# Kernel tuning notes

Hardware: AMD Instinct MI355X
Metric: run time of the kernel (lower is better)

Reference implementation:

```python
import jax, jax.numpy as jnp
import numpy as np

B, S, DIM = 8, 4096, 1024
DIM_LATENT = 1024
DEPTH = 2
NUM_LATENTS = 64
MAX_SEQ = 4096
DIM_HEAD = 64
HEADS = max(max(DIM, DIM_LATENT) // DIM_HEAD, 1)  # 16
INNER = HEADS * DIM_HEAD                           # 1024
HIDDEN = 4 * DIM_LATENT
LN_EPS = 1e-5
RMS_EPS = 1e-8


def setup_inputs() -> dict:
    key = jax.random.key(0)
    ks = jax.random.split(key, 10)
    return {
        "x": jax.random.normal(ks[0], (B, S, DIM), jnp.float32),
        "mask": jnp.ones((B, S), dtype=bool),
        "pos_table": jax.random.normal(ks[1], (MAX_SEQ, DIM), jnp.float32) * 0.02,
        "latents0": jax.random.normal(ks[2], (NUM_LATENTS, DIM_LATENT), jnp.float32) * 0.02,
        "ln_x_g": jnp.ones((DEPTH, DIM), jnp.float32),
        "ln_x_b": jnp.zeros((DEPTH, DIM), jnp.float32),
        "ln_l_g": jnp.ones((DEPTH, DIM_LATENT), jnp.float32),
        "ln_l_b": jnp.zeros((DEPTH, DIM_LATENT), jnp.float32),
        "qn_g": jnp.ones((DEPTH, DIM_HEAD), jnp.float32),
        "kn_g": jnp.ones((DEPTH, DIM_HEAD), jnp.float32),
        "Wq": jax.random.normal(ks[3], (DEPTH, DIM_LATENT, INNER), jnp.float32) * 0.02,
        "Wkv": jax.random.normal(ks[4], (DEPTH, DIM, 2 * INNER), jnp.float32) * 0.02,
        "Wo": jax.random.normal(ks[5], (DEPTH, INNER, DIM_LATENT), jnp.float32) * 0.02,
        "bo": jnp.zeros((DEPTH, DIM_LATENT), jnp.float32),
        "ff_ln_g": jnp.ones((DEPTH, DIM_LATENT), jnp.float32),
        "ff_ln_b": jnp.zeros((DEPTH, DIM_LATENT), jnp.float32),
        "W1": jax.random.normal(ks[6], (DEPTH, DIM_LATENT, HIDDEN), jnp.float32) * 0.02,
        "b1": jnp.zeros((DEPTH, HIDDEN), jnp.float32),
        "W2": jax.random.normal(ks[7], (DEPTH, HIDDEN, DIM_LATENT), jnp.float32) * 0.02,
        "b2": jnp.zeros((DEPTH, DIM_LATENT), jnp.float32),
        "fn_g": jnp.ones((DIM_LATENT,), jnp.float32),
        "fn_b": jnp.zeros((DIM_LATENT,), jnp.float32),
    }


def _ln(x, g, b):
    m = jnp.mean(x, axis=-1, keepdims=True)
    v = jnp.mean(jnp.square(x - m), axis=-1, keepdims=True)
    return (x - m) * jax.lax.rsqrt(v + LN_EPS) * g + b


def _rms(x, g):
    # torch RMSNorm: x / clamp(||x|| * d^-0.5, eps) * gamma
    n = jnp.sqrt(jnp.sum(jnp.square(x), axis=-1, keepdims=True)) * (DIM_HEAD ** -0.5)
    return x / jnp.maximum(n, RMS_EPS) * g


def reference(x, mask, pos_table, latents0, ln_x_g, ln_x_b, ln_l_g, ln_l_b,
              qn_g, kn_g, Wq, Wkv, Wo, bo, ff_ln_g, ff_ln_b, W1, b1, W2, b2,
              fn_g, fn_b):
    b, s, _ = x.shape
    x = x + pos_table[:s][None]                       # abs pos emb
    lat = jnp.broadcast_to(latents0, (b, NUM_LATENTS, DIM_LATENT))
    scale = DIM_HEAD ** -0.5
    pad_mask = jnp.concatenate(
        [mask, jnp.ones((b, NUM_LATENTS), dtype=bool)], axis=1)  # [b, s+nl]
    for i in range(DEPTH):
        xn = _ln(x, ln_x_g[i], ln_x_b[i])
        ln_lat = _ln(lat, ln_l_g[i], ln_l_b[i])
        # queries from latents
        q = (ln_lat @ Wq[i]).reshape(b, NUM_LATENTS, HEADS, DIM_HEAD)
        q = q.transpose(0, 2, 1, 3)                   # b h i d
        # kv from context + latents (dim == dim_latent -> shared to_kv)
        kv = jnp.concatenate([xn @ Wkv[i], ln_lat @ Wkv[i]], axis=1)
        n_kv = s + NUM_LATENTS
        kv = kv.reshape(b, n_kv, 2, HEADS, DIM_HEAD)
        k = kv[:, :, 0].transpose(0, 2, 1, 3)         # b h j d
        v = kv[:, :, 1].transpose(0, 2, 1, 3)
        sim = jnp.einsum('bhid,bhjd->bhij', _rms(q, qn_g[i]) * scale,
                         _rms(k, kn_g[i]))
        neg = -jnp.finfo(sim.dtype).max
        sim = jnp.where(pad_mask[:, None, None, :], sim, neg)
        attn = jax.nn.softmax(sim.astype(jnp.float32), axis=-1).astype(sim.dtype)
        out = jnp.einsum('bhij,bhjd->bhid', attn, v)
        out = out.transpose(0, 2, 1, 3).reshape(b, NUM_LATENTS, INNER)
        lat = out @ Wo[i] + bo[i] + lat               # attn residual
        h = _ln(lat, ff_ln_g[i], ff_ln_b[i]) @ W1[i] + b1[i]
        lat = jax.nn.gelu(h, approximate=False) @ W2[i] + b2[i] + lat  # ff residual
    return _ln(lat, fn_g, fn_b)
```

## Files before the change

### kernel.cpp

```cpp
#include <hip/hip_runtime.h>
#include <cstdint>
#include <cstddef>

typedef __bf16 bf16_t;
typedef __bf16 bf16x8 __attribute__((ext_vector_type(8)));
typedef float  f32x4  __attribute__((ext_vector_type(4)));

#define LN_EPS_F 1e-5f
#define RMS_EPS_F 1e-8f

static __device__ __forceinline__ void async_load16(const void* src, void* dst_lds) {
  __builtin_amdgcn_global_load_lds(
      (__attribute__((address_space(1))) void*)src,
      (__attribute__((address_space(3))) void*)dst_lds, 16, 0, 0);
}

static __device__ __forceinline__ unsigned short f2bfu(float f) {
  union { bf16_t h; unsigned short u; } cv;
  cv.h = (bf16_t)f;
  return cv.u;
}

__global__ __launch_bounds__(256)
void wconv_kernel(const float* __restrict__ src, bf16_t* __restrict__ dst, int K, int N) {
  __shared__ float t[32][33];
  int k0 = blockIdx.x * 32, n0 = blockIdx.y * 32;
  int tx = threadIdx.x & 31, ty = threadIdx.x >> 5;
  for (int r = ty; r < 32; r += 8)
    t[r][tx] = src[(size_t)(k0 + r) * N + n0 + tx];
  __syncthreads();
  for (int r = ty; r < 32; r += 8)
    dst[(size_t)(n0 + r) * K + k0 + tx] = (bf16_t)t[tx][r];
}

__global__ __launch_bounds__(256)
void ln_kernel(const float* __restrict__ X, const float* __restrict__ pos,
               const float* __restrict__ g, const float* __restrict__ bb,
               void* __restrict__ outp, int out_bf16) {
  int row = blockIdx.x, tid = threadIdx.x;
  int lane = tid & 63, wave = tid >> 6;
  float4 v = *(const float4*)(X + (size_t)row * 1024 + tid * 4);
  if (pos) {
    float4 p = *(const float4*)(pos + (size_t)(row & 4095) * 1024 + tid * 4);
    v.x += p.x; v.y += p.y; v.z += p.z; v.w += p.w;
  }
  float s1 = v.x + v.y + v.z + v.w;
  float s2 = v.x * v.x + v.y * v.y + v.z * v.z + v.w * v.w;
  for (int off = 32; off > 0; off >>= 1) {
    s1 += __shfl_xor(s1, off);
    s2 += __shfl_xor(s2, off);
  }
  __shared__ float red1[4], red2[4];
  if (lane == 0) { red1[wave] = s1; red2[wave] = s2; }
  __syncthreads();
  float S1 = red1[0] + red1[1] + red1[2] + red1[3];
  float S2 = red2[0] + red2[1] + red2[2] + red2[3];
  float mean = S1 * (1.0f / 1024.0f);
  float var  = S2 * (1.0f / 1024.0f) - mean * mean;
  float inv  = rsqrtf(var + LN_EPS_F);
  float4 gg  = *(const float4*)(g + tid * 4);
  float4 bb4 = *(const float4*)(bb + tid * 4);
  float y0 = (v.x - mean) * inv * gg.x + bb4.x;
  float y1 = (v.y - mean) * inv * gg.y + bb4.y;
  float y2 = (v.z - mean) * inv * gg.z + bb4.z;
  float y3 = (v.w - mean) * inv * gg.w + bb4.w;
  if (out_bf16) {
    ushort4 u; u.x = f2bfu(y0); u.y = f2bfu(y1); u.z = f2bfu(y2); u.w = f2bfu(y3);
    *(ushort4*)((bf16_t*)outp + (size_t)row * 1024 + tid * 4) = u;
  } else {
    float4 o; o.x = y0; o.y = y1; o.z = y2; o.w = y3;
    *(float4*)((float*)outp + (size_t)row * 1024 + tid * 4) = o;
  }
}

#define BAR() do { asm volatile("" ::: "memory"); __builtin_amdgcn_s_barrier(); asm volatile("" ::: "memory"); } while (0)
#define VMW(n_) asm volatile("s_waitcnt vmcnt(" #n_ ")" ::: "memory")

__global__ __launch_bounds__(512, 2)
void gemm256_kv(const bf16_t* __restrict__ A, const bf16_t* __restrict__ Bt,
                bf16_t* __restrict__ kbuf, bf16_t* __restrict__ vt,
                float* __restrict__ knsc, int K) {
  __shared__ __align__(16) bf16_t smem[65536];
  const int tid = threadIdx.x;
  const int lane = tid & 63, wave = tid >> 6;
  const int l15 = lane & 15, quad = lane >> 4;
  const int orig = blockIdx.x;
  const int xcd = orig & 7, pp_ = orig >> 3;
  const int m0 = (xcd * 16 + (pp_ >> 3)) * 256;
  const int n0 = (pp_ & 7) * 256;
  const int wm = (wave >> 2) * 128, wn = (wave & 3) * 64;

  const int r0 = wave * 16 + (lane >> 2);
  const int c0 = ((lane & 3) - (r0 >> 1)) & 3;
  const bf16_t* gA = A + (size_t)(m0 + r0) * K + c0 * 8;
  const bf16_t* gB = Bt + (size_t)(n0 + r0) * K + c0 * 8;

#define STG(t_, slot_) do {                                                    \
    const bf16_t* a_ = gA + (size_t)(t_) * 32;                                 \
    const bf16_t* b_ = gB + (size_t)(t_) * 32;                                 \
    bf16_t* d_ = smem + (slot_) * 16384 + wave * 512;                          \
    async_load16(a_, d_);                                                      \
    async_load16(a_ + (size_t)128 * K, d_ + 4096);                             \
    async_load16(b_, d_ + 8192);                                               \
    async_load16(b_ + (size_t)128 * K, d_ + 12288);                            \
  } while (0)

  const int rot = ((quad + (l15 >> 1)) & 3) << 3;
  const int offA0 = (wm + l15) * 32 + rot;
  const int offB0 = 8192 + (wn + l15) * 32 + rot;

  f32x4 acc[8][4];
  const f32x4 zero = {0.f, 0.f, 0.f, 0.f};
#pragma unroll
  for (int i = 0; i < 8; ++i)
#pragma unroll
    for (int j = 0; j < 4; ++j) acc[i][j] = zero;

  bf16x8 a[8], b[4], c[4];

#define ITER(t_, CUR, NXT) do {                                                \
    { int ts_ = (t_) + 3; if (ts_ > KT - 1) ts_ = KT - 1;                      \
      STG(ts_, ts_ & 3); }                                                     \
    const bf16_t* ns_ = smem + (((t_) + 1) & 3) * 16384;                       \
    _Pragma("unroll")                                                          \
    for (int mi = 0; mi < 8; ++mi) {                                           \
      _Pragma("unroll")                                                        \
      for (int ni = 0; ni < 4; ++ni)                                           \
        acc[mi][ni] = __builtin_amdgcn_mfma_f32_16x16x32_bf16(a[mi], CUR[ni], acc[mi][ni], 0, 0, 0); \
      a[mi] = *(const bf16x8*)(ns_ + offA0 + mi * 512);                        \
      if (mi < 4) NXT[mi] = *(const bf16x8*)(ns_ + offB0 + mi * 512);          \
    }                                                                          \
    VMW(4); BAR();                                                             \
  } while (0)

#define FCOMP(CUR) do {                                                        \
    _Pragma("unroll")                                                          \
    for (int mi = 0; mi < 8; ++mi)                                             \
      _Pragma("unroll")                                                        \
      for (int ni = 0; ni < 4; ++ni)                                           \
        acc[mi][ni] = __builtin_amdgcn_mfma_f32_16x16x32_bf16(a[mi], CUR[ni], acc[mi][ni], 0, 0, 0); \
  } while (0)

  const int KT = K >> 5;
  STG(0, 0); STG(1, 1); STG(2, 2);
  VMW(4); BAR();
#pragma unroll
  for (int mi = 0; mi < 8; ++mi) a[mi] = *(const bf16x8*)(smem + offA0 + mi * 512);
#pragma unroll
  for (int ni = 0; ni < 4; ++ni) b[ni] = *(const bf16x8*)(smem + offB0 + ni * 512);

  int t = 0;
  for (; t + 1 < KT - 1; t += 2) {
    ITER(t, b, c);
    ITER(t + 1, c, b);
  }
  ITER(t, b, c);
  FCOMP(c);
  __syncthreads();

  const int bq = m0 >> 12;
  const bool is_v = (n0 >= 1024);
  const int colbase = is_v ? (n0 - 1024) : n0;
  const int h = (colbase + wn) >> 6;
  const int bh = bq * 16 + h;
  const int j0w = (m0 & 4095) + wm;
  bf16_t* bnc = smem + wave * 8192;

  if (!is_v) {
#pragma unroll
    for (int mi = 0; mi < 8; ++mi) {
#pragma unroll
      for (int rg = 0; rg < 4; ++rg) {
        float tt = acc[mi][0][rg] * acc[mi][0][rg] + acc[mi][1][rg] * acc[mi][1][rg]
                 + acc[mi][2][rg] * acc[mi][2][rg] + acc[mi][3][rg] * acc[mi][3][rg];
        tt += __shfl_xor(tt, 1); tt += __shfl_xor(tt, 2);
        tt += __shfl_xor(tt, 4); tt += __shfl_xor(tt, 8);
        if (l15 == 0) {
          int jj = j0w + mi * 16 + quad * 4 + rg;
          knsc[(size_t)bh * 4160 + jj] = 1.0f / fmaxf(sqrtf(tt) * 0.125f, RMS_EPS_F);
        }
      }
    }
#pragma unroll
    for (int mi = 0; mi < 8; ++mi)
#pragma unroll
      for (int ni = 0; ni < 4; ++ni)
#pragma unroll
        for (int rg = 0; rg < 4; ++rg)
          bnc[(mi * 16 + quad * 4 + rg) * 64 + ni * 16 + l15] = (bf16_t)acc[mi][ni][rg];
#pragma unroll
    for (int p = 0; p < 16; ++p) {
      int e = p * 64 + lane;
      int jr = e >> 3, cq = e & 7;
      bf16x8 vl = *(const bf16x8*)&bnc[jr * 64 + cq * 8];
      *(bf16x8*)(kbuf + ((size_t)bh * 4160 + j0w + jr) * 64 + cq * 8) = vl;
    }
  } else {
#pragma unroll
    for (int mi = 0; mi < 8; ++mi)
#pragma unroll
      for (int ni = 0; ni < 4; ++ni) {
        ushort4 u;
        u.x = f2bfu(acc[mi][ni].x); u.y = f2bfu(acc[mi][ni].y);
        u.z = f2bfu(acc[mi][ni].z); u.w = f2bfu(acc[mi][ni].w);
        *(ushort4*)&bnc[(ni * 16 + l15) * 128 + mi * 16 + quad * 4] = u;
      }
#pragma unroll
    for (int p = 0; p < 16; ++p) {
      int e = p * 64 + lane;
      int dr = e >> 4, cq = e & 15;
      bf16x8 vl = *(const bf16x8*)&bnc[dr * 128 + cq * 8];
      *(bf16x8*)(vt + ((size_t)bh * 64 + dr) * 4160 + j0w + cq * 8) = vl;
    }
  }
#undef STG
#undef ITER
#undef FCOMP
}

__global__ __launch_bounds__(256)
void gemm64_bt(const bf16_t* __restrict__ A, const bf16_t* __restrict__ Bt,
               float* __restrict__ C, int K, int lda, int ldb, int ldc,
               int zdiv, long long aO, long long aI, long long bO, long long bI,
               long long cO, long long cI) {
  __shared__ __align__(16) bf16_t As[64 * 32];
  __shared__ __align__(16) bf16_t Bs[64 * 32];
  const int tid = threadIdx.x;
  const int lane = tid & 63, wave = tid >> 6;
  const int z = blockIdx.z;
  const int zh = z / zdiv, zl = z - zh * zdiv;
  const bf16_t* Ab = A + zh * aO + zl * aI;
  const bf16_t* Bb = Bt + zh * bO + zl * bI;
  float* Cb = C + zh * cO + zl * cI;
  const int m0 = blockIdx.x * 64, n0 = blockIdx.y * 64;
  const int wm = (wave >> 1) * 32, wn = (wave & 1) * 32;
  const int l15 = lane & 15, quad = lane >> 4;

  f32x4 acc[2][2];
  const f32x4 zero = {0.f, 0.f, 0.f, 0.f};
  acc[0][0] = zero; acc[0][1] = zero; acc[1][0] = zero; acc[1][1] = zero;

  const int ebase = wave * 64;
  const int e = ebase + lane;
  const int row = e >> 2, c = e & 3;
  for (int kb = 0; kb < K; kb += 32) {
    async_load16(Ab + (size_t)(m0 + row) * lda + kb + c * 8, &As[ebase * 8]);
    async_load16(Bb + (size_t)(n0 + row) * ldb + kb + c * 8, &Bs[ebase * 8]);
    __syncthreads();
    bf16x8 a0 = *(const bf16x8*)&As[(wm + l15) * 32 + quad * 8];
    bf16x8 a1 = *(const bf16x8*)&As[(wm + 16 + l15) * 32 + quad * 8];
    bf16x8 b0 = *(const bf16x8*)&Bs[(wn + l15) * 32 + quad * 8];
    bf16x8 b1 = *(const bf16x8*)&Bs[(wn + 16 + l15) * 32 + quad * 8];
    acc[0][0] = __builtin_amdgcn_mfma_f32_16x16x32_bf16(a0, b0, acc[0][0], 0, 0, 0);
    acc[0][1] = __builtin_amdgcn_mfma_f32_16x16x32_bf16(a0, b1, acc[0][1], 0, 0, 0);
    acc[1][0] = __builtin_amdgcn_mfma_f32_16x16x32_bf16(a1, b0, acc[1][0], 0, 0, 0);
    acc[1][1] = __builtin_amdgcn_mfma_f32_16x16x32_bf16(a1, b1, acc[1][1], 0, 0, 0);
    __syncthreads();
  }
#pragma unroll
  for (int mi = 0; mi < 2; ++mi) {
    int r0 = m0 + wm + mi * 16 + quad * 4;
#pragma unroll
    for (int ni = 0; ni < 2; ++ni) {
      int col = n0 + wn + ni * 16 + l15;
      float* p = Cb + (size_t)r0 * ldc + col;
      p[0] = acc[mi][ni].x;
      p[(size_t)ldc] = acc[mi][ni].y;
      p[(size_t)ldc * 2] = acc[mi][ni].z;
      p[(size_t)ldc * 3] = acc[mi][ni].w;
    }
  }
}

__global__ __launch_bounds__(256)
void rms_q_kernel(const float* __restrict__ q, const float* __restrict__ gq,
                  const float* __restrict__ gk, bf16_t* __restrict__ outp) {
  int gw = blockIdx.x * 4 + (threadIdx.x >> 6);
  int lane = threadIdx.x & 63;
  float x = q[(size_t)gw * 64 + lane];
  float ss = x * x;
  for (int off = 32; off > 0; off >>= 1) ss += __shfl_xor(ss, off);
  float n = sqrtf(ss) * 0.125f;
  outp[(size_t)gw * 64 + lane] =
      (bf16_t)(x / fmaxf(n, RMS_EPS_F) * gq[lane] * gk[lane] * 0.125f);
}

__global__ __launch_bounds__(256)
void prep_lat_kernel(const float* __restrict__ kvlat, float* __restrict__ knsc,
                     bf16_t* __restrict__ kbuf, bf16_t* __restrict__ vt) {
  int gw = blockIdx.x * 4 + (threadIdx.x >> 6);
  int lane = threadIdx.x & 63;
  int rowi = gw >> 4, h = gw & 15;
  int b = rowi >> 6, il = rowi & 63;
  float kx = kvlat[(size_t)rowi * 2048 + h * 64 + lane];
  float vx = kvlat[(size_t)rowi * 2048 + 1024 + h * 64 + lane];
  float ss = kx * kx;
  for (int off = 32; off > 0; off >>= 1) ss += __shfl_xor(ss, off);
  int bh = b * 16 + h, j = 4096 + il;
  kbuf[((size_t)bh * 4160 + j) * 64 + lane] = (bf16_t)kx;
  if (lane == 0)
    knsc[(size_t)bh * 4160 + j] = 1.0f / fmaxf(sqrtf(ss) * 0.125f, RMS_EPS_F);
  vt[((size_t)bh * 64 + lane) * 4160 + j] = (bf16_t)vx;
}

__global__ __launch_bounds__(256)
void flash_kernel(const bf16_t* __restrict__ qrms, const bf16_t* __restrict__ kbuf,
                  const bf16_t* __restrict__ vt, const float* __restrict__ knsc,
                  float* __restrict__ Opart, float* __restrict__ mpart,
                  float* __restrict__ lpart) {
  __shared__ __align__(16) bf16_t Qs[4096];
  __shared__ __align__(16) bf16_t Ks[4096];
  __shared__ __align__(16) bf16_t Vs[4096];
  __shared__ __align__(16) bf16_t Ps[4 * 16 * 72];
  __shared__ float kss[64];
  const int tid = threadIdx.x, lane = tid & 63, wave = tid >> 6;
  const int l15 = lane & 15, quad = lane >> 4;
  const int bh = blockIdx.z, ch = blockIdx.x;
  const int b = bh >> 4, h = bh & 15;

#pragma unroll
  for (int p = 0; p < 2; ++p) {
    int eb = p * 256 + wave * 64;
    int e = eb + lane;
    int i = e >> 3, q = e & 7;
    async_load16(qrms + (size_t)b * 65536 + (size_t)i * 1024 + h * 64 + ((q ^ (i & 7)) * 8),
                 &Qs[eb * 8]);
  }
  __syncthreads();
  bf16x8 qf[2];
#pragma unroll
  for (int kk = 0; kk < 2; ++kk)
    qf[kk] = *(const bf16x8*)&Qs[(wave * 16 + l15) * 64 + (((kk * 4 + quad) ^ (l15 & 7)) * 8)];

  float m_i[4], l_i[4];
  f32x4 O[4];
  const f32x4 zero = {0.f, 0.f, 0.f, 0.f};
#pragma unroll
  for (int rg = 0; rg < 4; ++rg) { m_i[rg] = -3.0e38f; l_i[rg] = 0.f; }
#pragma unroll
  for (int nd = 0; nd < 4; ++nd) O[nd] = zero;

  for (int t = 0; t < 5; ++t) {
    const int j0 = ch * 320 + t * 64;
    __syncthreads();
#pragma unroll
    for (int p = 0; p < 2; ++p) {
      int eb = p * 256 + wave * 64;
      int e = eb + lane;
      int rj = e >> 3, q = e & 7;
      async_load16(kbuf + ((size_t)bh * 4160 + j0 + rj) * 64 + ((q ^ (rj & 7)) * 8),
                   &Ks[eb * 8]);
      async_load16(vt + ((size_t)bh * 64 + rj) * 4160 + j0 + ((q ^ (rj & 7)) * 8),
                   &Vs[eb * 8]);
    }
    if (tid < 64) kss[tid] = knsc[(size_t)bh * 4160 + j0 + tid];
    __syncthreads();

    f32x4 s[4];
#pragma unroll
    for (int ni = 0; ni < 4; ++ni) s[ni] = zero;
#pragma unroll
    for (int kk = 0; kk < 2; ++kk) {
#pragma unroll
      for (int ni = 0; ni < 4; ++ni) {
        bf16x8 bv = *(const bf16x8*)&Ks[(ni * 16 + l15) * 64 + (((kk * 4 + quad) ^ (l15 & 7)) * 8)];
        s[ni] = __builtin_amdgcn_mfma_f32_16x16x32_bf16(qf[kk], bv, s[ni], 0, 0, 0);
      }
    }
#pragma unroll
    for (int ni = 0; ni < 4; ++ni) {
      float cs = kss[ni * 16 + l15];
      s[ni].x *= cs; s[ni].y *= cs; s[ni].z *= cs; s[ni].w *= cs;
    }
    float al[4];
#pragma unroll
    for (int rg = 0; rg < 4; ++rg) {
      float tm = fmaxf(fmaxf(s[0][rg], s[1][rg]), fmaxf(s[2][rg], s[3][rg]));
      tm = fmaxf(tm, __shfl_xor(tm, 1)); tm = fmaxf(tm, __shfl_xor(tm, 2));
      tm = fmaxf(tm, __shfl_xor(tm, 4)); tm = fmaxf(tm, __shfl_xor(tm, 8));
      float mn = fmaxf(m_i[rg], tm);
      al[rg] = __expf(m_i[rg] - mn);
      m_i[rg] = mn;
    }
    float rs[4] = {0.f, 0.f, 0.f, 0.f};
#pragma unroll
    for (int ni = 0; ni < 4; ++ni) {
#pragma unroll
      for (int rg = 0; rg < 4; ++rg) {
        float pv = __expf(s[ni][rg] - m_i[rg]);
        s[ni][rg] = pv;
        rs[rg] += pv;
        Ps[wave * 1152 + (quad * 4 + rg) * 72 + ni * 16 + l15] = (bf16_t)pv;
      }
    }
#pragma unroll
    for (int rg = 0; rg < 4; ++rg) {
      float t2 = rs[rg];
      t2 += __shfl_xor(t2, 1); t2 += __shfl_xor(t2, 2);
      t2 += __shfl_xor(t2, 4); t2 += __shfl_xor(t2, 8);
      l_i[rg] = l_i[rg] * al[rg] + t2;
    }
#pragma unroll
    for (int nd = 0; nd < 4; ++nd) {
      O[nd].x *= al[0]; O[nd].y *= al[1]; O[nd].z *= al[2]; O[nd].w *= al[3];
    }
#pragma unroll
    for (int kk2 = 0; kk2 < 2; ++kk2) {
      bf16x8 af = *(const bf16x8*)&Ps[wave * 1152 + l15 * 72 + kk2 * 32 + quad * 8];
#pragma unroll
      for (int nd = 0; nd < 4; ++nd) {
        bf16x8 bv = *(const bf16x8*)&Vs[(nd * 16 + l15) * 64 + (((kk2 * 4 + quad) ^ (l15 & 7)) * 8)];
        O[nd] = __builtin_amdgcn_mfma_f32_16x16x32_bf16(af, bv, O[nd], 0, 0, 0);
      }
    }
  }
  const size_t obase = (size_t)(ch * 128 + bh) * 64;
#pragma unroll
  for (int nd = 0; nd < 4; ++nd) {
    int colb = nd * 16 + l15;
#pragma unroll
    for (int rg = 0; rg < 4; ++rg) {
      int rowi = wave * 16 + quad * 4 + rg;
      Opart[(obase + rowi) * 64 + colb] = O[nd][rg];
    }
  }
  if (l15 == 0) {
#pragma unroll
    for (int rg = 0; rg < 4; ++rg) {
      int rowi = wave * 16 + quad * 4 + rg;
      mpart[obase + rowi] = m_i[rg];
      lpart[obase + rowi] = l_i[rg];
    }
  }
}

__global__ __launch_bounds__(256)
void combine_kernel(const float* __restrict__ Opart, const float* __restrict__ mpart,
                    const float* __restrict__ lpart, bf16_t* __restrict__ obf) {
  const int bh = blockIdx.z, xi = blockIdx.x;
  const int wave = threadIdx.x >> 6, lane = threadIdx.x & 63;
  const int b = bh >> 4, h = bh & 15;
  for (int ii = 0; ii < 4; ++ii) {
    int i = xi * 16 + ii * 4 + wave;
    float mv[13];
    float M = -3.0e38f;
#pragma unroll
    for (int c = 0; c < 13; ++c) {
      mv[c] = mpart[(size_t)(c * 128 + bh) * 64 + i];
      M = fmaxf(M, mv[c]);
    }
    float L = 0.f, acc = 0.f;
#pragma unroll
    for (int c = 0; c < 13; ++c) {
      float e = __expf(mv[c] - M);
      L += e * lpart[(size_t)(c * 128 + bh) * 64 + i];
      acc += e * Opart[((size_t)(c * 128 + bh) * 64 + i) * 64 + lane];
    }
    obf[(size_t)b * 65536 + (size_t)i * 1024 + h * 64 + lane] = (bf16_t)(acc / L);
  }
}

__global__ __launch_bounds__(256)
void lat_init_kernel(const float* __restrict__ l0, float* __restrict__ lat) {
  size_t i = (size_t)blockIdx.x * 256 + threadIdx.x;
  lat[i] = l0[i & 65535];
}
__global__ __launch_bounds__(256)
void resid_kernel(float* __restrict__ lat, const float* __restrict__ add,
                  const float* __restrict__ bias) {
  size_t i = (size_t)blockIdx.x * 256 + threadIdx.x;
  lat[i] += add[i] + bias[i & 1023];
}
__global__ __launch_bounds__(256)
void resid4_kernel(float* __restrict__ lat, const float* __restrict__ cs,
                   const float* __restrict__ bias) {
  size_t i = (size_t)blockIdx.x * 256 + threadIdx.x;
  lat[i] += bias[i & 1023] + cs[i] + cs[i + 524288] + cs[i + 1048576] + cs[i + 1572864];
}
__global__ __launch_bounds__(256)
void gelu_kernel(const float* __restrict__ h, const float* __restrict__ b1,
                 bf16_t* __restrict__ o) {
  size_t i = (size_t)blockIdx.x * 256 + threadIdx.x;
  float x = h[i] + b1[i & 4095];
  o[i] = (bf16_t)(0.5f * x * (1.0f + erff(x * 0.70710678118654752f)));
}

extern "C" void kernel_launch(void* const* d_in, const int* in_sizes, int n_in,
                              void* d_out, int out_size, void* d_ws, size_t ws_size,
                              hipStream_t stream) {
  const float* x      = (const float*)d_in[0];
  const float* pos    = (const float*)d_in[2];
  const float* lat0   = (const float*)d_in[3];
  const float* ln_x_g = (const float*)d_in[4];
  const float* ln_x_b = (const float*)d_in[5];
  const float* ln_l_g = (const float*)d_in[6];
  const float* ln_l_b = (const float*)d_in[7];
  const float* qn_g   = (const float*)d_in[8];
  const float* kn_g   = (const float*)d_in[9];
  const float* Wq     = (const float*)d_in[10];
  const float* Wkv    = (const float*)d_in[11];
  const float* Wo     = (const float*)d_in[12];
  const float* bo     = (const float*)d_in[13];
  const float* ffln_g = (const float*)d_in[14];
  const float* ffln_b = (const float*)d_in[15];
  const float* W1     = (const float*)d_in[16];
  const float* b1     = (const float*)d_in[17];
  const float* W2     = (const float*)d_in[18];
  const float* b2     = (const float*)d_in[19];
  const float* fn_g   = (const float*)d_in[20];
  const float* fn_b   = (const float*)d_in[21];
  (void)in_sizes; (void)n_in; (void)out_size; (void)ws_size;

  char* base = (char*)d_ws;
  size_t off = 0;
  auto alloc = [&](size_t bytes) -> void* {
    void* p = base + off;
    off += (bytes + 255) & ~(size_t)255;
    return p;
  };
  bf16_t* Wqt   = (bf16_t*)alloc(2ull * 1024 * 1024 * 2);
  bf16_t* Wkvt  = (bf16_t*)alloc(2ull * 2048 * 1024 * 2);
  bf16_t* Wot   = (bf16_t*)alloc(2ull * 1024 * 1024 * 2);
  bf16_t* W1t   = (bf16_t*)alloc(2ull * 4096 * 1024 * 2);
  bf16_t* W2t   = (bf16_t*)alloc(2ull * 1024 * 4096 * 2);
  bf16_t* xn    = (bf16_t*)alloc(32768ull * 1024 * 2);
  bf16_t* kbuf  = (bf16_t*)alloc(128ull * 4160 * 64 * 2);
  bf16_t* vt    = (bf16_t*)alloc(128ull * 64 * 4160 * 2);
  float*  knsc  = (float*)alloc(128ull * 4160 * 4);
  float*  Opart = (float*)alloc(13ull * 128 * 64 * 64 * 4);
  float*  mpart = (float*)alloc(13ull * 128 * 64 * 4);
  float*  lpart = (float*)alloc(13ull * 128 * 64 * 4);
  float*  lat   = (float*)alloc(512ull * 1024 * 4);
  bf16_t* lnl   = (bf16_t*)alloc(512ull * 1024 * 2);
  float*  qbuf  = (float*)alloc(512ull * 1024 * 4);
  bf16_t* qrms  = (bf16_t*)alloc(512ull * 1024 * 2);
  float*  kvlat = (float*)alloc(512ull * 2048 * 4);
  bf16_t* obf   = (bf16_t*)alloc(512ull * 1024 * 2);
  float*  oW    = (float*)alloc(512ull * 1024 * 4);
  float*  ffh   = (float*)alloc(512ull * 4096 * 4);
  bf16_t* ffgb  = (bf16_t*)alloc(512ull * 4096 * 2);
  float*  ffo   = (float*)alloc(512ull * 1024 * 4);
  (void)ffo;

  for (int i = 0; i < 2; ++i) {
    wconv_kernel<<<dim3(32, 32), 256, 0, stream>>>(Wq  + (size_t)i * 1024 * 1024, Wqt  + (size_t)i * 1024 * 1024, 1024, 1024);
    wconv_kernel<<<dim3(32, 64), 256, 0, stream>>>(Wkv + (size_t)i * 1024 * 2048, Wkvt + (size_t)i * 2048 * 1024, 1024, 2048);
    wconv_kernel<<<dim3(32, 32), 256, 0, stream>>>(Wo  + (size_t)i * 1024 * 1024, Wot  + (size_t)i * 1024 * 1024, 1024, 1024);
    wconv_kernel<<<dim3(32, 128), 256, 0, stream>>>(W1 + (size_t)i * 1024 * 4096, W1t + (size_t)i * 4096 * 1024, 1024, 4096);
    wconv_kernel<<<dim3(128, 32), 256, 0, stream>>>(W2 + (size_t)i * 4096 * 1024, W2t + (size_t)i * 1024 * 4096, 4096, 1024);
  }
  lat_init_kernel<<<2048, 256, 0, stream>>>(lat0, lat);

  for (int i = 0; i < 2; ++i) {
    ln_kernel<<<32768, 256, 0, stream>>>(x, pos, ln_x_g + i * 1024, ln_x_b + i * 1024, xn, 1);
    gemm256_kv<<<dim3(1024), dim3(512), 0, stream>>>(xn, Wkvt + (size_t)i * 2048 * 1024, kbuf, vt, knsc, 1024);
    ln_kernel<<<512, 256, 0, stream>>>(lat, nullptr, ln_l_g + i * 1024, ln_l_b + i * 1024, lnl, 1);
    gemm64_bt<<<dim3(8, 16, 1), 256, 0, stream>>>(lnl, Wqt + (size_t)i * 1024 * 1024, qbuf,
        1024, 1024, 1024, 1024, 1, 0, 0, 0, 0, 0, 0);
    gemm64_bt<<<dim3(8, 32, 1), 256, 0, stream>>>(lnl, Wkvt + (size_t)i * 2048 * 1024, kvlat,
        1024, 1024, 1024, 2048, 1, 0, 0, 0, 0, 0, 0);
    rms_q_kernel<<<2048, 256, 0, stream>>>(qbuf, qn_g + i * 64, kn_g + i * 64, qrms);
    prep_lat_kernel<<<2048, 256, 0, stream>>>(kvlat, knsc, kbuf, vt);
    flash_kernel<<<dim3(13, 1, 128), 256, 0, stream>>>(qrms, kbuf, vt, knsc, Opart, mpart, lpart);
    combine_kernel<<<dim3(4, 1, 128), 256, 0, stream>>>(Opart, mpart, lpart, obf);
    gemm64_bt<<<dim3(8, 16, 1), 256, 0, stream>>>(obf, Wot + (size_t)i * 1024 * 1024, oW,
        1024, 1024, 1024, 1024, 1, 0, 0, 0, 0, 0, 0);
    resid_kernel<<<2048, 256, 0, stream>>>(lat, oW, bo + i * 1024);
    ln_kernel<<<512, 256, 0, stream>>>(lat, nullptr, ffln_g + i * 1024, ffln_b + i * 1024, lnl, 1);
    gemm64_bt<<<dim3(8, 64, 1), 256, 0, stream>>>(lnl, W1t + (size_t)i * 4096 * 1024, ffh,
        1024, 1024, 1024, 4096, 1, 0, 0, 0, 0, 0, 0);
    gelu_kernel<<<8192, 256, 0, stream>>>(ffh, b1 + i * 4096, ffgb);
    gemm64_bt<<<dim3(8, 16, 4), 256, 0, stream>>>(ffgb, W2t + (size_t)i * 1024 * 4096, ffh,
        1024, 4096, 4096, 1024, 4, 0, 1024, 0, 1024, 0, 524288);
    resid4_kernel<<<2048, 256, 0, stream>>>(lat, ffh, b2 + i * 1024);
  }
  ln_kernel<<<512, 256, 0, stream>>>(lat, nullptr, fn_g, fn_b, d_out, 0);
}
```

Before: 1.035 ms.

## Load KV GEMM B operand straight from global into registers, halve LDS

The KV projection GEMM now stages only the A tile through LDS. Each wave loads its B fragments directly from global memory into registers one k-step ahead, and the pipeline is restructured around this. The change halves shared memory per block, and the epilogue is split into two halves with an XOR-swizzled LDS layout to fit the smaller buffer and avoid bank conflicts. In exchange, B is fetched redundantly from global by the waves that share it, and global-load latency for B is now exposed more directly.

```diff
diff --git a/kernel.cpp b/kernel.cpp
--- a/kernel.cpp
+++ b/kernel.cpp
@@ -80,7 +80,7 @@
 void gemm256_kv(const bf16_t* __restrict__ A, const bf16_t* __restrict__ Bt,
                 bf16_t* __restrict__ kbuf, bf16_t* __restrict__ vt,
                 float* __restrict__ knsc, int K) {
-  __shared__ __align__(16) bf16_t smem[65536];
+  __shared__ __align__(16) bf16_t smem[32768];
   const int tid = threadIdx.x;
   const int lane = tid & 63, wave = tid >> 6;
   const int l15 = lane & 15, quad = lane >> 4;
@@ -93,21 +93,24 @@
   const int r0 = wave * 16 + (lane >> 2);
   const int c0 = ((lane & 3) - (r0 >> 1)) & 3;
   const bf16_t* gA = A + (size_t)(m0 + r0) * K + c0 * 8;
-  const bf16_t* gB = Bt + (size_t)(n0 + r0) * K + c0 * 8;
 
 #define STG(t_, slot_) do {                                                    \
     const bf16_t* a_ = gA + (size_t)(t_) * 32;                                 \
-    const bf16_t* b_ = gB + (size_t)(t_) * 32;                                 \
-    bf16_t* d_ = smem + (slot_) * 16384 + wave * 512;                          \
+    bf16_t* d_ = smem + (slot_) * 8192 + wave * 512;                           \
     async_load16(a_, d_);                                                      \
     async_load16(a_ + (size_t)128 * K, d_ + 4096);                             \
-    async_load16(b_, d_ + 8192);                                               \
-    async_load16(b_ + (size_t)128 * K, d_ + 12288);                            \
   } while (0)
 
   const int rot = ((quad + (l15 >> 1)) & 3) << 3;
   const int offA0 = (wm + l15) * 32 + rot;
-  const int offB0 = 8192 + (wn + l15) * 32 + rot;
+
+  const bf16_t* gBf = Bt + (size_t)(n0 + wn + l15) * K + quad * 8;
+
+#define BLD(t_, R_) do {                                                       \
+    _Pragma("unroll")                                                          \
+    for (int ni = 0; ni < 4; ++ni)                                             \
+      R_[ni] = *(const bf16x8*)(gBf + (size_t)ni * 16 * K + (size_t)(t_) * 32);\
+  } while (0)
 
   f32x4 acc[8][4];
   const f32x4 zero = {0.f, 0.f, 0.f, 0.f};
@@ -118,22 +121,10 @@
 
   bf16x8 a[8], b[4], c[4];
 
-#define ITER(t_, CUR, NXT) do {                                                \
-    { int ts_ = (t_) + 3; if (ts_ > KT - 1) ts_ = KT - 1;                      \
-      STG(ts_, ts_ & 3); }                                                     \
-    const bf16_t* ns_ = smem + (((t_) + 1) & 3) * 16384;                       \
+#define COMP(slot_, CUR) do {                                                  \
+    const bf16_t* sb_ = smem + (slot_) * 8192;                                 \
     _Pragma("unroll")                                                          \
-    for (int mi = 0; mi < 8; ++mi) {                                           \
-      _Pragma("unroll")                                                        \
-      for (int ni = 0; ni < 4; ++ni)                                           \
-        acc[mi][ni] = __builtin_amdgcn_mfma_f32_16x16x32_bf16(a[mi], CUR[ni], acc[mi][ni], 0, 0, 0); \
-      a[mi] = *(const bf16x8*)(ns_ + offA0 + mi * 512);                        \
-      if (mi < 4) NXT[mi] = *(const bf16x8*)(ns_ + offB0 + mi * 512);          \
-    }                                                                          \
-    VMW(4); BAR();                                                             \
-  } while (0)
-
-#define FCOMP(CUR) do {                                                        \
+    for (int mi = 0; mi < 8; ++mi) a[mi] = *(const bf16x8*)(sb_ + offA0 + mi * 512); \
     _Pragma("unroll")                                                          \
     for (int mi = 0; mi < 8; ++mi)                                             \
       _Pragma("unroll")                                                        \
@@ -141,13 +132,19 @@
         acc[mi][ni] = __builtin_amdgcn_mfma_f32_16x16x32_bf16(a[mi], CUR[ni], acc[mi][ni], 0, 0, 0); \
   } while (0)
 
+#define ITER(t_, CUR, NXT) do {                                                \
+    BLD((t_) + 1, NXT);                                                        \
+    { int ts_ = (t_) + 3; if (ts_ > KT - 1) ts_ = KT - 1;                      \
+      STG(ts_, ((t_) + 3) & 3); }                                              \
+    COMP((t_) & 3, CUR);                                                       \
+    __builtin_amdgcn_sched_barrier(0);                                         \
+    VMW(8); BAR();                                                             \
+  } while (0)
+
   const int KT = K >> 5;
   STG(0, 0); STG(1, 1); STG(2, 2);
+  BLD(0, b);
   VMW(4); BAR();
-#pragma unroll
-  for (int mi = 0; mi < 8; ++mi) a[mi] = *(const bf16x8*)(smem + offA0 + mi * 512);
-#pragma unroll
-  for (int ni = 0; ni < 4; ++ni) b[ni] = *(const bf16x8*)(smem + offB0 + ni * 512);
 
   int t = 0;
   for (; t + 1 < KT - 1; t += 2) {
@@ -155,7 +152,7 @@
     ITER(t + 1, c, b);
   }
   ITER(t, b, c);
-  FCOMP(c);
+  COMP((KT - 1) & 3, c);
   __syncthreads();
 
   const int bq = m0 >> 12;
@@ -164,7 +161,7 @@
   const int h = (colbase + wn) >> 6;
   const int bh = bq * 16 + h;
   const int j0w = (m0 & 4095) + wm;
-  bf16_t* bnc = smem + wave * 8192;
+  bf16_t* bnc = smem + wave * 4096;
 
   if (!is_v) {
 #pragma unroll
@@ -182,40 +179,60 @@
       }
     }
 #pragma unroll
-    for (int mi = 0; mi < 8; ++mi)
-#pragma unroll
-      for (int ni = 0; ni < 4; ++ni)
-#pragma unroll
-        for (int rg = 0; rg < 4; ++rg)
-          bnc[(mi * 16 + quad * 4 + rg) * 64 + ni * 16 + l15] = (bf16_t)acc[mi][ni][rg];
-#pragma unroll
-    for (int p = 0; p < 16; ++p) {
-      int e = p * 64 + lane;
-      int jr = e >> 3, cq = e & 7;
-      bf16x8 vl = *(const bf16x8*)&bnc[jr * 64 + cq * 8];
-      *(bf16x8*)(kbuf + ((size_t)bh * 4160 + j0w + jr) * 64 + cq * 8) = vl;
+    for (int half = 0; half < 2; ++half) {
+      if (half) __syncthreads();
+#pragma unroll
+      for (int mi = 0; mi < 4; ++mi) {
+        int mg = half * 4 + mi;
+#pragma unroll
+        for (int ni = 0; ni < 4; ++ni) {
+          int g = ni * 2 + (l15 >> 3);
+#pragma unroll
+          for (int rg = 0; rg < 4; ++rg) {
+            int j = mi * 16 + quad * 4 + rg;
+            bnc[j * 64 + (((g ^ (j & 7)) << 3) | (l15 & 7))] = (bf16_t)acc[mg][ni][rg];
+          }
+        }
+      }
+#pragma unroll
+      for (int p = 0; p < 8; ++p) {
+        int e = p * 64 + lane;
+        int jr = e >> 3, cq = e & 7;
+        bf16x8 vl = *(const bf16x8*)&bnc[jr * 64 + ((cq ^ (jr & 7)) << 3)];
+        *(bf16x8*)(kbuf + ((size_t)bh * 4160 + j0w + half * 64 + jr) * 64 + cq * 8) = vl;
+      }
     }
   } else {
 #pragma unroll
-    for (int mi = 0; mi < 8; ++mi)
-#pragma unroll
-      for (int ni = 0; ni < 4; ++ni) {
-        ushort4 u;
-        u.x = f2bfu(acc[mi][ni].x); u.y = f2bfu(acc[mi][ni].y);
-        u.z = f2bfu(acc[mi][ni].z); u.w = f2bfu(acc[mi][ni].w);
-        *(ushort4*)&bnc[(ni * 16 + l15) * 128 + mi * 16 + quad * 4] = u;
-      }
-#pragma unroll
-    for (int p = 0; p < 16; ++p) {
-      int e = p * 64 + lane;
-      int dr = e >> 4, cq = e & 15;
-      bf16x8 vl = *(const bf16x8*)&bnc[dr * 128 + cq * 8];
-      *(bf16x8*)(vt + ((size_t)bh * 64 + dr) * 4160 + j0w + cq * 8) = vl;
+    for (int half = 0; half < 2; ++half) {
+      if (half) __syncthreads();
+#pragma unroll
+      for (int mi = 0; mi < 4; ++mi) {
+        int mg = half * 4 + mi;
+        int g = mi * 2 + (quad >> 1);
+        int wi = (quad & 1) * 4;
+#pragma unroll
+        for (int ni = 0; ni < 4; ++ni) {
+          int row = ni * 16 + l15;
+          ushort4 u;
+          u.x = f2bfu(acc[mg][ni].x); u.y = f2bfu(acc[mg][ni].y);
+          u.z = f2bfu(acc[mg][ni].z); u.w = f2bfu(acc[mg][ni].w);
+          *(ushort4*)&bnc[row * 64 + (((g ^ (row & 7)) << 3) | wi)] = u;
+        }
+      }
+#pragma unroll
+      for (int p = 0; p < 8; ++p) {
+        int e = p * 64 + lane;
+        int dr = e >> 3, cq = e & 7;
+        bf16x8 vl = *(const bf16x8*)&bnc[dr * 64 + ((cq ^ (dr & 7)) << 3)];
+        *(bf16x8*)(vt + ((size_t)bh * 64 + dr) * 4160 + j0w + half * 64 + cq * 8) = vl;
+      }
     }
   }
 #undef STG
+#undef BLD
+#undef COMP
 #undef ITER
-#undef FCOMP
 }
 
 __global__ __launch_bounds__(256)
```

New measurement: 1.160 ms. 12.0% more time.
